# Kernel tuning notes

Hardware: AMD Instinct MI355X
Metric: run time of the kernel (lower is better)

## Reference

```python
import jax, jax.numpy as jnp
import numpy as np

N = 10000  # num_users + num_posts


def gcn_conv(x, edge_index, W, b):
    """PyG-style GCNConv: out = D^-1/2 (A+I) D^-1/2 (x W) + b."""
    h = x @ W  # [N, d]
    src, dst = edge_index[0], edge_index[1]
    loop = jnp.arange(N, dtype=src.dtype)
    src = jnp.concatenate([src, loop])
    dst = jnp.concatenate([dst, loop])
    ones = jnp.ones(src.shape[0], dtype=h.dtype)
    deg = jax.ops.segment_sum(ones, dst, num_segments=N)  # in-degree incl. self-loop
    dinv = jnp.where(deg > 0, jax.lax.rsqrt(deg), 0.0)
    norm = dinv[src] * dinv[dst]  # [E+N]
    msg = h[src] * norm[:, None]  # gather + scale
    out = jax.ops.segment_sum(msg, dst, num_segments=N)  # scatter-add
    return out + b


def setup_inputs() -> dict:
    key = jax.random.key(0)
    k1, k2, k3, k4 = jax.random.split(key, 4)
    E = 320000
    H = 64
    x = jax.random.normal(k1, (N, N), dtype=jnp.float32)
    edge_index = jax.random.randint(k2, (2, E), 0, N, dtype=jnp.int64)
    W1 = jax.random.normal(k3, (N, H), dtype=jnp.float32) / np.sqrt(N)
    b1 = jnp.zeros((H,), dtype=jnp.float32)
    W2 = jax.random.normal(k4, (H, H), dtype=jnp.float32) / np.sqrt(H)
    b2 = jnp.zeros((H,), dtype=jnp.float32)
    return {"x": x, "edge_index": edge_index, "W1": W1, "b1": b1, "W2": W2, "b2": b2}


def reference(x, edge_index, W1, b1, W2, b2):
    h = gcn_conv(x, edge_index, W1, b1)
    h = jax.nn.relu(h)
    return gcn_conv(h, edge_index, W2, b2)
```

## Files before the change

### kernel.cpp

```cpp
#include <hip/hip_runtime.h>
#include <hip/hip_bf16.h>

#define NND 10000
#define HD 64
#define KPAD 10112
#define ROWS 64
#define RBLK 157
#define NCHUNK 3
#define KCHUNK 3456
#define KSTEP 128
#define KHEAD 5632
#define CAP 96
#define ABYTES 32768
#define BBYTES 16384
#define BUFB (ABYTES + BBYTES)

typedef __attribute__((ext_vector_type(8))) short bf16x8;
typedef __attribute__((ext_vector_type(4))) float f32x4;

__device__ __forceinline__ short f2bf(float f) {
    unsigned u = __builtin_bit_cast(unsigned, f);
    u += 0x7FFFu + ((u >> 16) & 1u);
    return (short)(u >> 16);
}

__device__ __forceinline__ void gload16(const void* gp, void* lp) {
    __builtin_amdgcn_global_load_lds(
        (const __attribute__((address_space(1))) unsigned int*)gp,
        (__attribute__((address_space(3))) unsigned int*)lp, 16, 0, 0);
}

__device__ __forceinline__ void gload16nt(const void* gp, void* lp) {
    __builtin_amdgcn_global_load_lds(
        (const __attribute__((address_space(1))) unsigned int*)gp,
        (__attribute__((address_space(3))) unsigned int*)lp, 16, 0, 2);
}

__global__ __launch_bounds__(256) void prep2_kernel(const float* __restrict__ W1,
        int* __restrict__ cnt, float* __restrict__ h, short* __restrict__ w1t) {
    __shared__ float tile[64][65];
    const int t = threadIdx.x;
    const int k0 = blockIdx.x * 64;
    #pragma unroll
    for (int i = 0; i < 16; ++i) {
        int r = i * 4 + (t >> 6);
        int c = t & 63;
        int k = k0 + r;
        tile[r][c] = (k < NND) ? W1[(size_t)k * HD + c] : 0.f;
    }
    __syncthreads();
    #pragma unroll
    for (int i = 0; i < 16; ++i) {
        int c = i * 4 + (t >> 6);
        int k = t & 63;
        if (k0 + k < KPAD)
            w1t[(size_t)c * KPAD + k0 + k] = f2bf(tile[k][c]);
    }
    int tid = blockIdx.x * 256 + t;
    if (tid < NND) cnt[tid] = 0;
    f32x4* h4 = (f32x4*)h;
    f32x4 z = {0.f, 0.f, 0.f, 0.f};
    #pragma unroll
    for (int i = 0; i < 4; ++i) {
        int idx = tid + i * 40448;
        if (idx < NND * HD / 4) h4[idx] = z;
    }
}

__global__ __launch_bounds__(1024, 1) void csrgemm1_kernel(const float* __restrict__ x,
        const short* __restrict__ w1t, float* __restrict__ h,
        const int* __restrict__ ei, int* __restrict__ cnt, int* __restrict__ csr, int E) {
    {
        const int stride = RBLK * NCHUNK * 1024;
        for (int e = blockIdx.x * 1024 + threadIdx.x; e < E; e += stride) {
            int s = ei[e], d = ei[E + e];
            int pos = atomicAdd(&cnt[d], 1);
            if (pos < CAP) csr[d * CAP + pos] = s;
        }
    }
    asm volatile("s_waitcnt vmcnt(0)" ::: "memory");
    __shared__ f32x4 smem4[3 * BUFB / 16];
    char* smem = (char*)smem4;
    const int l = threadIdx.x & 63;
    const int w = threadIdx.x >> 6;
    const int r0 = (blockIdx.x / NCHUNK) * ROWS;
    const int kstart = (blockIdx.x % NCHUNK) * KCHUNK;
    const int kend = min(KPAD, kstart + KCHUNK);
    const int nsteps = (kend - kstart) >> 7;

    const int wr = (w & 3) * 16;
    const int wc = (w >> 2) * 16;
    const int akg = l >> 4;
    const int l15 = l & 15;
    const int l7 = l & 7;

    f32x4 acc = {0.f, 0.f, 0.f, 0.f};

    union AFU { bf16x8 v; __hip_bfloat162 p[4]; };

    auto stage = [&](int buf, int k0) {
        char* sb = smem + buf * BUFB;
        const bool cached = (k0 < KHEAD);
        #pragma unroll
        for (int i = 0; i < 2; ++i) {
            int row = w * 4 + i * 2 + (l >> 5);
            int rg = r0 + row; if (rg >= NND) rg = 0;
            int pl = ((l & 31) >> 1) ^ (row & 7);
            const char* gp = (const char*)x + (size_t)rg * (NND * 4)
                             + (size_t)k0 * 4 + pl * 32 + (l & 1) * 16;
            if (k0 + pl * 8 + (l & 1) * 4 + 3 >= NND)
                gp = (const char*)x;
            if (cached) gload16(gp, sb + w * 2048 + i * 1024);
            else        gload16nt(gp, sb + w * 2048 + i * 1024);
        }
        {
            int col = w * 4 + (l >> 4);
            int cl = (l & 15) ^ (col & 7);
            const char* gp = (const char*)w1t + (size_t)col * (KPAD * 2)
                             + (size_t)k0 * 2 + cl * 16;
            gload16(gp, sb + ABYTES + w * 1024);
        }
    };

    stage(0, kstart);
    if (nsteps > 1) stage(1, kstart + KSTEP);
    for (int t = 0; t < nsteps; ++t) {
        if (t + 1 < nsteps) asm volatile("s_waitcnt vmcnt(3)" ::: "memory");
        else                asm volatile("s_waitcnt vmcnt(0)" ::: "memory");
        __builtin_amdgcn_s_barrier();
        if (t + 2 < nsteps) stage((t + 2) % 3, kstart + (t + 2) * KSTEP);
        const char* sb = smem + (t % 3) * BUFB;
        #pragma unroll
        for (int ks = 0; ks < 4; ++ks) {
            int cp = (ks * 4 + akg) ^ l7;
            int arow = wr + l15;
            const char* ap = sb + arow * 512 + cp * 32;
            f32x4 a0 = *(const f32x4*)ap;
            f32x4 a1 = *(const f32x4*)(ap + 16);
            AFU af;
            af.p[0] = __float22bfloat162_rn(float2{a0[0], a0[1]});
            af.p[1] = __float22bfloat162_rn(float2{a0[2], a0[3]});
            af.p[2] = __float22bfloat162_rn(float2{a1[0], a1[1]});
            af.p[3] = __float22bfloat162_rn(float2{a1[2], a1[3]});
            int col = wc + l15;
            bf16x8 b = *(const bf16x8*)(sb + ABYTES + col * 256 + cp * 16);
            acc = __builtin_amdgcn_mfma_f32_16x16x32_bf16(af.v, b, acc, 0, 0, 0);
        }
    }
    {
        const int crow = r0 + wr + akg * 4;
        const int ccol = wc + l15;
        #pragma unroll
        for (int j = 0; j < 4; ++j) {
            int row = crow + j;
            if (row < NND)
                unsafeAtomicAdd(&h[(size_t)row * HD + ccol], acc[j]);
        }
    }
}

__global__ __launch_bounds__(256) void scale_h_kernel(float* __restrict__ h,
        const int* __restrict__ cnt) {
    const int wave = threadIdx.x >> 6, lane = threadIdx.x & 63;
    const int r = blockIdx.x * 4 + wave;
    if (r >= NND) return;
    const float dd = rsqrtf((float)(min(cnt[r], CAP) + 1));
    h[(size_t)r * HD + lane] *= dd;
}

__global__ __launch_bounds__(256) void agg1g2_kernel(const float* __restrict__ h,
        const int* __restrict__ csr, const int* __restrict__ cnt,
        const float* __restrict__ b1, const float* __restrict__ W2,
        float* __restrict__ h2) {
    __shared__ float w2s[HD * HD];
    __shared__ float rowbuf[4][HD];
    for (int i = threadIdx.x; i < HD * HD; i += 256) w2s[i] = W2[i];
    const int wave = threadIdx.x >> 6, lane = threadIdx.x & 63;
    const int d = blockIdx.x * 4 + wave;
    const int n = min(cnt[d], CAP);
    const float dd = rsqrtf((float)(n + 1));
    float t0 = h[(size_t)d * HD + lane];
    float t1 = 0.f, t2 = 0.f, t3 = 0.f, t4 = 0.f, t5 = 0.f, t6 = 0.f, t7 = 0.f;
    const int* row = csr + d * CAP;
    int j = 0;
    for (; j + 16 <= n; j += 16) {
        int a0 = row[j],    a1 = row[j+1],  a2 = row[j+2],  a3 = row[j+3];
        int a4 = row[j+4],  a5 = row[j+5],  a6 = row[j+6],  a7 = row[j+7];
        int a8 = row[j+8],  a9 = row[j+9],  aa = row[j+10], ab = row[j+11];
        int ac = row[j+12], ad = row[j+13], ae = row[j+14], af = row[j+15];
        t0 += h[(size_t)a0 * HD + lane];  t1 += h[(size_t)a1 * HD + lane];
        t2 += h[(size_t)a2 * HD + lane];  t3 += h[(size_t)a3 * HD + lane];
        t4 += h[(size_t)a4 * HD + lane];  t5 += h[(size_t)a5 * HD + lane];
        t6 += h[(size_t)a6 * HD + lane];  t7 += h[(size_t)a7 * HD + lane];
        t0 += h[(size_t)a8 * HD + lane];  t1 += h[(size_t)a9 * HD + lane];
        t2 += h[(size_t)aa * HD + lane];  t3 += h[(size_t)ab * HD + lane];
        t4 += h[(size_t)ac * HD + lane];  t5 += h[(size_t)ad * HD + lane];
        t6 += h[(size_t)ae * HD + lane];  t7 += h[(size_t)af * HD + lane];
    }
    for (; j + 8 <= n; j += 8) {
        int a0 = row[j],   a1 = row[j+1], a2 = row[j+2], a3 = row[j+3];
        int a4 = row[j+4], a5 = row[j+5], a6 = row[j+6], a7 = row[j+7];
        t0 += h[(size_t)a0 * HD + lane];  t1 += h[(size_t)a1 * HD + lane];
        t2 += h[(size_t)a2 * HD + lane];  t3 += h[(size_t)a3 * HD + lane];
        t4 += h[(size_t)a4 * HD + lane];  t5 += h[(size_t)a5 * HD + lane];
        t6 += h[(size_t)a6 * HD + lane];  t7 += h[(size_t)a7 * HD + lane];
    }
    for (; j < n; ++j) t0 += h[(size_t)row[j] * HD + lane];
    float sum = ((t0 + t1) + (t2 + t3)) + ((t4 + t5) + (t6 + t7));
    float acc = fmaf(sum, dd, b1[lane]);
    rowbuf[wave][lane] = fmaxf(acc, 0.f);
    __syncthreads();
    float s = 0.f;
    #pragma unroll
    for (int k = 0; k < HD; ++k)
        s = fmaf(rowbuf[wave][k], w2s[k * HD + lane], s);
    h2[(size_t)d * HD + lane] = s * dd;
}

__global__ __launch_bounds__(256) void agg2_kernel(const float* __restrict__ feat,
        const int* __restrict__ csr, const int* __restrict__ cnt,
        const float* __restrict__ bias, float* __restrict__ out) {
    const int wave = threadIdx.x >> 6, lane = threadIdx.x & 63;
    const int d = blockIdx.x * 4 + wave;
    const int n = min(cnt[d], CAP);
    const float dd = rsqrtf((float)(n + 1));
    float t0 = feat[(size_t)d * HD + lane];
    float t1 = 0.f, t2 = 0.f, t3 = 0.f, t4 = 0.f, t5 = 0.f, t6 = 0.f, t7 = 0.f;
    const int* row = csr + d * CAP;
    int j = 0;
    for (; j + 16 <= n; j += 16) {
        int a0 = row[j],    a1 = row[j+1],  a2 = row[j+2],  a3 = row[j+3];
        int a4 = row[j+4],  a5 = row[j+5],  a6 = row[j+6],  a7 = row[j+7];
        int a8 = row[j+8],  a9 = row[j+9],  aa = row[j+10], ab = row[j+11];
        int ac = row[j+12], ad = row[j+13], ae = row[j+14], af = row[j+15];
        t0 += feat[(size_t)a0 * HD + lane];  t1 += feat[(size_t)a1 * HD + lane];
        t2 += feat[(size_t)a2 * HD + lane];  t3 += feat[(size_t)a3 * HD + lane];
        t4 += feat[(size_t)a4 * HD + lane];  t5 += feat[(size_t)a5 * HD + lane];
        t6 += feat[(size_t)a6 * HD + lane];  t7 += feat[(size_t)a7 * HD + lane];
        t0 += feat[(size_t)a8 * HD + lane];  t1 += feat[(size_t)a9 * HD + lane];
        t2 += feat[(size_t)aa * HD + lane];  t3 += feat[(size_t)ab * HD + lane];
        t4 += feat[(size_t)ac * HD + lane];  t5 += feat[(size_t)ad * HD + lane];
        t6 += feat[(size_t)ae * HD + lane];  t7 += feat[(size_t)af * HD + lane];
    }
    for (; j + 8 <= n; j += 8) {
        int a0 = row[j],   a1 = row[j+1], a2 = row[j+2], a3 = row[j+3];
        int a4 = row[j+4], a5 = row[j+5], a6 = row[j+6], a7 = row[j+7];
        t0 += feat[(size_t)a0 * HD + lane];  t1 += feat[(size_t)a1 * HD + lane];
        t2 += feat[(size_t)a2 * HD + lane];  t3 += feat[(size_t)a3 * HD + lane];
        t4 += feat[(size_t)a4 * HD + lane];  t5 += feat[(size_t)a5 * HD + lane];
        t6 += feat[(size_t)a6 * HD + lane];  t7 += feat[(size_t)a7 * HD + lane];
    }
    for (; j < n; ++j) t0 += feat[(size_t)row[j] * HD + lane];
    float sum = ((t0 + t1) + (t2 + t3)) + ((t4 + t5) + (t6 + t7));
    out[(size_t)d * HD + lane] = fmaf(sum, dd, bias[lane]);
}

extern "C" void kernel_launch(void* const* d_in, const int* in_sizes, int n_in,
                              void* d_out, int out_size, void* d_ws, size_t ws_size,
                              hipStream_t stream) {
    const float* x  = (const float*)d_in[0];
    const int*   ei = (const int*)d_in[1];
    const float* W1 = (const float*)d_in[2];
    const float* b1 = (const float*)d_in[3];
    const float* W2 = (const float*)d_in[4];
    const float* b2 = (const float*)d_in[5];
    float* out = (float*)d_out;
    const int E = in_sizes[1] / 2;

    char* ws = (char*)d_ws;
    int*   cnt  = (int*)(ws);
    float* h    = (float*)(ws + 40000);
    float* h2   = (float*)(ws + 2600000);
    short* w1t  = (short*)(ws + 5160000);
    int*   csr  = (int*)(ws + 6454336);

    prep2_kernel<<<158, 256, 0, stream>>>(W1, cnt, h, w1t);
    csrgemm1_kernel<<<RBLK * NCHUNK, 1024, 0, stream>>>(x, w1t, h, ei, cnt, csr, E);
    scale_h_kernel<<<2500, 256, 0, stream>>>(h, cnt);
    agg1g2_kernel<<<2500, 256, 0, stream>>>(h, csr, cnt, b1, W2, h2);
    agg2_kernel<<<2500, 256, 0, stream>>>(h2, csr, cnt, b2, out);
}
```

Baseline: 134.2 us.

## Use 512-thread blocks with two MFMA tiles per wave and balanced split-K grid

Halves the GEMM block size to 8 waves, each computing a 16x32 output tile with two MFMAs that share one converted A fragment. This cuts redundant fp32-to-bf16 conversion and LDS A reads per MFMA. The launch goes from 471 blocks to exactly 512 by giving the first 41 row groups 4 K-chunks and the rest 3, so the split-K work spreads more evenly over the CUs. Each wave now issues twice as many loads per stage, the wait count rises to match, and there are more atomic adds into h from the extra chunks.

```diff
diff --git a/kernel.cpp b/kernel.cpp
--- a/kernel.cpp
+++ b/kernel.cpp
@@ -6,14 +6,13 @@
 #define KPAD 10112
 #define ROWS 64
 #define RBLK 157
-#define NCHUNK 3
-#define KCHUNK 3456
 #define KSTEP 128
 #define KHEAD 5632
 #define CAP 96
 #define ABYTES 32768
 #define BBYTES 16384
 #define BUFB (ABYTES + BBYTES)
+#define GRID 512
 
 typedef __attribute__((ext_vector_type(8))) short bf16x8;
 typedef __attribute__((ext_vector_type(4))) float f32x4;
@@ -67,12 +66,12 @@
     }
 }
 
-__global__ __launch_bounds__(1024, 1) void csrgemm1_kernel(const float* __restrict__ x,
+__global__ __launch_bounds__(512, 1) void csrgemm1_kernel(const float* __restrict__ x,
         const short* __restrict__ w1t, float* __restrict__ h,
         const int* __restrict__ ei, int* __restrict__ cnt, int* __restrict__ csr, int E) {
     {
-        const int stride = RBLK * NCHUNK * 1024;
-        for (int e = blockIdx.x * 1024 + threadIdx.x; e < E; e += stride) {
+        const int stride = GRID * 512;
+        for (int e = blockIdx.x * 512 + threadIdx.x; e < E; e += stride) {
             int s = ei[e], d = ei[E + e];
             int pos = atomicAdd(&cnt[d], 1);
             if (pos < CAP) csr[d * CAP + pos] = s;
@@ -83,18 +82,26 @@
     char* smem = (char*)smem4;
     const int l = threadIdx.x & 63;
     const int w = threadIdx.x >> 6;
-    const int r0 = (blockIdx.x / NCHUNK) * ROWS;
-    const int kstart = (blockIdx.x % NCHUNK) * KCHUNK;
-    const int kend = min(KPAD, kstart + KCHUNK);
-    const int nsteps = (kend - kstart) >> 7;
+    int g, c, nch;
+    {
+        const int b = blockIdx.x;
+        if (b < 164) { g = b >> 2; c = b & 3; nch = 4; }
+        else { int bb = b - 164; int q = bb / 3; g = 41 + q; c = bb - q * 3; nch = 3; }
+    }
+    const int r0 = g * ROWS;
+    int kstart, nsteps;
+    if (nch == 4) { kstart = c * 20 * KSTEP; nsteps = (c == 3) ? 19 : 20; }
+    else          { kstart = c * 27 * KSTEP; nsteps = (c == 2) ? 25 : 27; }
 
     const int wr = (w & 3) * 16;
-    const int wc = (w >> 2) * 16;
+    const int wc = (w >> 2) * 32;
     const int akg = l >> 4;
     const int l15 = l & 15;
     const int l7 = l & 7;
 
-    f32x4 acc = {0.f, 0.f, 0.f, 0.f};
+    f32x4 acc[2];
+    acc[0] = f32x4{0.f, 0.f, 0.f, 0.f};
+    acc[1] = f32x4{0.f, 0.f, 0.f, 0.f};
 
     union AFU { bf16x8 v; __hip_bfloat162 p[4]; };
 
@@ -102,30 +109,31 @@
         char* sb = smem + buf * BUFB;
         const bool cached = (k0 < KHEAD);
         #pragma unroll
-        for (int i = 0; i < 2; ++i) {
-            int row = w * 4 + i * 2 + (l >> 5);
+        for (int i = 0; i < 4; ++i) {
+            int row = w * 8 + i * 2 + (l >> 5);
             int rg = r0 + row; if (rg >= NND) rg = 0;
             int pl = ((l & 31) >> 1) ^ (row & 7);
             const char* gp = (const char*)x + (size_t)rg * (NND * 4)
                              + (size_t)k0 * 4 + pl * 32 + (l & 1) * 16;
             if (k0 + pl * 8 + (l & 1) * 4 + 3 >= NND)
                 gp = (const char*)x;
-            if (cached) gload16(gp, sb + w * 2048 + i * 1024);
-            else        gload16nt(gp, sb + w * 2048 + i * 1024);
-        }
-        {
-            int col = w * 4 + (l >> 4);
+            if (cached) gload16(gp, sb + w * 4096 + i * 1024);
+            else        gload16nt(gp, sb + w * 4096 + i * 1024);
+        }
+        #pragma unroll
+        for (int j = 0; j < 2; ++j) {
+            int col = w * 8 + j * 4 + (l >> 4);
             int cl = (l & 15) ^ (col & 7);
             const char* gp = (const char*)w1t + (size_t)col * (KPAD * 2)
                              + (size_t)k0 * 2 + cl * 16;
-            gload16(gp, sb + ABYTES + w * 1024);
+            gload16(gp, sb + ABYTES + w * 2048 + j * 1024);
         }
     };
 
     stage(0, kstart);
     if (nsteps > 1) stage(1, kstart + KSTEP);
     for (int t = 0; t < nsteps; ++t) {
-        if (t + 1 < nsteps) asm volatile("s_waitcnt vmcnt(3)" ::: "memory");
+        if (t + 1 < nsteps) asm volatile("s_waitcnt vmcnt(6)" ::: "memory");
         else                asm volatile("s_waitcnt vmcnt(0)" ::: "memory");
         __builtin_amdgcn_s_barrier();
         if (t + 2 < nsteps) stage((t + 2) % 3, kstart + (t + 2) * KSTEP);
@@ -142,19 +150,25 @@
             af.p[1] = __float22bfloat162_rn(float2{a0[2], a0[3]});
             af.p[2] = __float22bfloat162_rn(float2{a1[0], a1[1]});
             af.p[3] = __float22bfloat162_rn(float2{a1[2], a1[3]});
-            int col = wc + l15;
-            bf16x8 b = *(const bf16x8*)(sb + ABYTES + col * 256 + cp * 16);
-            acc = __builtin_amdgcn_mfma_f32_16x16x32_bf16(af.v, b, acc, 0, 0, 0);
+            #pragma unroll
+            for (int cg = 0; cg < 2; ++cg) {
+                int col = wc + cg * 16 + l15;
+                bf16x8 b = *(const bf16x8*)(sb + ABYTES + col * 256 + cp * 16);
+                acc[cg] = __builtin_amdgcn_mfma_f32_16x16x32_bf16(af.v, b, acc[cg], 0, 0, 0);
+            }
         }
     }
     {
         const int crow = r0 + wr + akg * 4;
-        const int ccol = wc + l15;
-        #pragma unroll
-        for (int j = 0; j < 4; ++j) {
-            int row = crow + j;
-            if (row < NND)
-                unsafeAtomicAdd(&h[(size_t)row * HD + ccol], acc[j]);
+        #pragma unroll
+        for (int cg = 0; cg < 2; ++cg) {
+            const int ccol = wc + cg * 16 + l15;
+            #pragma unroll
+            for (int j = 0; j < 4; ++j) {
+                int row = crow + j;
+                if (row < NND)
+                    unsafeAtomicAdd(&h[(size_t)row * HD + ccol], acc[cg][j]);
+            }
         }
     }
 }
@@ -275,7 +289,7 @@
     int*   csr  = (int*)(ws + 6454336);
 
     prep2_kernel<<<158, 256, 0, stream>>>(W1, cnt, h, w1t);
-    csrgemm1_kernel<<<RBLK * NCHUNK, 1024, 0, stream>>>(x, w1t, h, ei, cnt, csr, E);
+    csrgemm1_kernel<<<GRID, 512, 0, stream>>>(x, w1t, h, ei, cnt, csr, E);
     scale_h_kernel<<<2500, 256, 0, stream>>>(h, cnt);
     agg1g2_kernel<<<2500, 256, 0, stream>>>(h, csr, cnt, b1, W2, h2);
     agg2_kernel<<<2500, 256, 0, stream>>>(h2, csr, cnt, b2, out);
```

New measurement: 128.3 us (median of 2 runs). -4.3%, faster.
